# Optimization experiments

Hardware: AMD Instinct MI355X
Metric: run time of the kernel (lower is better)

The kernel has to match this reference:

```python
import jax, jax.numpy as jnp
import numpy as np

# DeepSeek MLA prefill pipeline (absorbed form), matching the GEMM/bmm/sparse-attention
# Dims: m=512 tokens, hidden=7168, d_kv_c=512, d_q_c=1536, d_r=64, d_q=d_kv=128,
# h=16 local heads, attention dim d = d_kv_c + d_r = 576, s_kv=4096, topk=512.

M, HID = 512, 7168
D_KV_C, D_Q_C, D_R, D_Q, D_KV = 512, 1536, 64, 128, 128
H = 16
S_KV, TOPK = 4096, 512
D_ATT = D_KV_C + D_R  # 576


def setup_inputs() -> dict:
    key = jax.random.key(0)
    ks = jax.random.split(key, 8)
    s = lambda n: 1.0 / np.sqrt(n).astype(np.float32)
    return {
        "x": jax.random.normal(ks[0], (M, HID), jnp.float32),
        "W_cqkv": jax.random.normal(ks[1], (HID, D_KV_C + D_Q_C + D_R), jnp.float32) * s(HID),
        "W_uq": jax.random.normal(ks[2], (D_Q_C, H * (D_Q + D_R)), jnp.float32) * s(D_Q_C),
        "W_qk": jax.random.normal(ks[3], (H, D_Q, D_KV_C), jnp.float32) * s(D_Q),
        "kv_cache": jax.random.normal(ks[4], (S_KV, D_ATT), jnp.float32),
        "W_o1": jax.random.normal(ks[5], (H, D_KV_C, D_KV), jnp.float32) * s(D_KV_C),
        "W_oproj": jax.random.normal(ks[6], (H * D_KV, HID), jnp.float32) * s(H * D_KV),
        "indices": jax.random.randint(ks[7], (M, TOPK), 0, S_KV, jnp.int32),
    }


def reference(x, W_cqkv, W_uq, W_qk, kv_cache, W_o1, W_oproj, indices):
    # 1) QKV compression GEMM: [m, hid] @ [hid, d_kv_c + d_q_c + d_r]
    c = x @ W_cqkv
    kv_c_new = c[:, :D_KV_C]                      # compressed KV (would extend cache)
    q_c = c[:, D_KV_C:D_KV_C + D_Q_C]             # [m, d_q_c]
    # (kv_c_new / k_r_new feed the cache in a real pipeline; attention below reads

    # 2) Q uncompression GEMM: [m, d_q_c] @ [d_q_c, h*(d_q+d_r)]
    q = (q_c @ W_uq).reshape(M, H, D_Q + D_R)
    q_nope, q_pe = q[..., :D_Q], q[..., D_Q:]     # [m,h,128], [m,h,64]

    # 3) Q absorb bmm: per-head [m, d_q] @ [d_q, d_kv_c]
    q_abs = jnp.einsum('mhq,hqc->mhc', q_nope, W_qk)
    q_full = jnp.concatenate([q_abs, q_pe], axis=-1)  # [m, h, 576]

    # 4) Top-k sparse MLA attention (flash_mla_sparse_fwd math):
    #    indices shared across heads (h_kv = 1); gather kv rows per query token.
    kv_g = kv_cache[indices]                      # [m, topk, 576]
    sm_scale = 1.0 / jnp.sqrt(jnp.float32(D_ATT))
    scores = jnp.einsum('mhd,mtd->mht', q_full, kv_g) * sm_scale
    attn = jax.nn.softmax(scores, axis=-1)        # [m, h, topk]
    o = jnp.einsum('mht,mtc->mhc', attn, kv_g[..., :D_KV_C])  # value = first d_kv_c dims

    # 5) O bmm: per-head [m, d_kv_c] @ [d_kv_c, d_kv]
    o2 = jnp.einsum('mhc,hcv->mhv', o, W_o1)      # [m, h, 128]

    # 6) O projection GEMM: [m, h*d_kv] @ [h*d_kv, hid]
    out = o2.reshape(M, H * D_KV) @ W_oproj       # [m, hid]
    return out
```

## Files before the change

kernel.cpp:

```cpp
#include <hip/hip_runtime.h>
#include <hip/hip_bf16.h>

#define M_DIM 512
#define HID 7168
#define D_KV_C 512
#define D_Q_C 1536
#define D_R 64
#define D_Q 128
#define D_KV 128
#define H_DIM 16
#define S_KV 4096
#define TOPK 512
#define D_ATT 576

typedef _Float16 half_t;
typedef __attribute__((ext_vector_type(8))) _Float16 f16x8_t;
typedef __attribute__((ext_vector_type(4))) float f32x4_t;
typedef __attribute__((ext_vector_type(2))) unsigned int u32x2_t;

#define MFMA_F16(a, b, c) __builtin_amdgcn_mfma_f32_16x16x32_f16((a), (b), (c), 0, 0, 0)

__device__ __forceinline__ unsigned lds_addr32(const void* p) {
    return (unsigned)(unsigned long long)(const __attribute__((address_space(3))) char*)p;
}

typedef const __attribute__((address_space(1))) unsigned int* gptr_t;
typedef __attribute__((address_space(3))) unsigned int* lptr_t;
__device__ __forceinline__ void gload_lds16(const void* g, void* l) {
    __builtin_amdgcn_global_load_lds((gptr_t)g, (lptr_t)l, 16, 0, 0);
}

__global__ __launch_bounds__(256) void cvt_f16(const float* __restrict__ src,
                                               half_t* __restrict__ dst, int n8)
{
    int i = blockIdx.x * 256 + threadIdx.x;
    if (i >= n8) return;
    const float4* s = (const float4*)src + (size_t)i * 2;
    float4 a = s[0], b = s[1];
    f16x8_t o;
    o[0] = (half_t)a.x; o[1] = (half_t)a.y; o[2] = (half_t)a.z; o[3] = (half_t)a.w;
    o[4] = (half_t)b.x; o[5] = (half_t)b.y; o[6] = (half_t)b.z; o[7] = (half_t)b.w;
    *(f16x8_t*)(dst + (size_t)i * 8) = o;
}

__global__ __launch_bounds__(256) void cvt_t(
    const float* __restrict__ src, int ld_src, long long sS,
    half_t* __restrict__ dst, int ld_dst, long long sD)
{
    src += (size_t)blockIdx.z * sS;
    dst += (size_t)blockIdx.z * sD;
    int k0 = blockIdx.y * 64, n0 = blockIdx.x * 64;
    __shared__ half_t t[64][80];
    int tid = threadIdx.x;
    int kr = tid >> 4, nc = (tid & 15) * 4;
    #pragma unroll
    for (int i = 0; i < 4; i++) {
        float4 v = *(const float4*)&src[(size_t)(k0 + kr + i * 16) * ld_src + n0 + nc];
        t[nc + 0][kr + i * 16] = (half_t)v.x;
        t[nc + 1][kr + i * 16] = (half_t)v.y;
        t[nc + 2][kr + i * 16] = (half_t)v.z;
        t[nc + 3][kr + i * 16] = (half_t)v.w;
    }
    __syncthreads();
    int nr = tid >> 2, kc = (tid & 3) * 16;
    f16x8_t w0 = *(const f16x8_t*)&t[nr][kc];
    f16x8_t w1 = *(const f16x8_t*)&t[nr][kc + 8];
    *(f16x8_t*)&dst[(size_t)(n0 + nr) * ld_dst + k0 + kc] = w0;
    *(f16x8_t*)&dst[(size_t)(n0 + nr) * ld_dst + k0 + kc + 8] = w1;
}

template<bool F16OUT>
__global__ __launch_bounds__(256) void gemm_f16t(
    const half_t* __restrict__ A, int lda, long long sA,
    const half_t* __restrict__ Bt, int ldb, long long sB,
    void* __restrict__ Cv, int ldc, long long sC, int K)
{
    A  += (size_t)blockIdx.z * sA;
    Bt += (size_t)blockIdx.z * sB;
    const int bm = blockIdx.y * 64, bn = blockIdx.x * 64;

    __shared__ __align__(16) char lds[2][16384];

    const int tid = threadIdx.x, w = tid >> 6, lane = tid & 63;
    const int l15 = lane & 15, q = lane >> 4;
    const int wr = w >> 1, wc = w & 1;

    const half_t* gA[2];
    const half_t* gB[2];
    #pragma unroll
    for (int p = 0; p < 2; p++) {
        int c = p * 64 + lane;
        int rl = c >> 3;
        int sg = (c & 7) ^ (rl & 7);
        gA[p] = A  + (size_t)(bm + w * 16 + rl) * lda + sg * 8;
        gB[p] = Bt + (size_t)(bn + w * 16 + rl) * ldb + sg * 8;
    }

    f32x4_t acc[2][2];
    #pragma unroll
    for (int i = 0; i < 2; i++)
        #pragma unroll
        for (int j = 0; j < 2; j++) acc[i][j] = (f32x4_t){0.f, 0.f, 0.f, 0.f};

    const int nsteps = K >> 6;

    {
        char* ab = lds[0];
        char* bb = ab + 8192;
        #pragma unroll
        for (int p = 0; p < 2; p++) {
            gload_lds16(gA[p], ab + w * 2048 + p * 1024);
            gload_lds16(gB[p], bb + w * 2048 + p * 1024);
        }
    }
    __syncthreads();

    int cur = 0;
    for (int s = 0; s < nsteps; s++) {
        if (s + 1 < nsteps) {
            int k0 = (s + 1) << 6;
            char* ab = lds[cur ^ 1];
            char* bb = ab + 8192;
            #pragma unroll
            for (int p = 0; p < 2; p++) {
                gload_lds16(gA[p] + k0, ab + w * 2048 + p * 1024);
                gload_lds16(gB[p] + k0, bb + w * 2048 + p * 1024);
            }
        }
        {
            const char* ab = lds[cur];
            const char* bb = ab + 8192;
            #pragma unroll
            for (int kk = 0; kk < 2; kk++) {
                f16x8_t av[2], bv[2];
                #pragma unroll
                for (int i = 0; i < 2; i++) {
                    int ra = wr * 32 + i * 16 + l15;
                    av[i] = *(const f16x8_t*)(ab + ra * 128 + (((kk * 4 + q) ^ (ra & 7)) * 16));
                    int rb = wc * 32 + i * 16 + l15;
                    bv[i] = *(const f16x8_t*)(bb + rb * 128 + (((kk * 4 + q) ^ (rb & 7)) * 16));
                }
                #pragma unroll
                for (int i = 0; i < 2; i++)
                    #pragma unroll
                    for (int j = 0; j < 2; j++)
                        acc[i][j] = MFMA_F16(av[i], bv[j], acc[i][j]);
            }
        }
        __syncthreads();
        cur ^= 1;
    }

    half_t* Ch = (half_t*)Cv + (F16OUT ? (size_t)blockIdx.z * sC : 0);
    float*  Cf = (float*)Cv  + (F16OUT ? 0 : (size_t)blockIdx.z * sC);
    #pragma unroll
    for (int i = 0; i < 2; i++)
        #pragma unroll
        for (int j = 0; j < 2; j++)
            #pragma unroll
            for (int r = 0; r < 4; r++) {
                size_t row = bm + wr * 32 + i * 16 + q * 4 + r;
                size_t col = bn + wc * 32 + j * 16 + l15;
                if (F16OUT) Ch[row * ldc + col] = (half_t)acc[i][j][r];
                else        Cf[row * ldc + col] = acc[i][j][r];
            }
}

__global__ void copy_pe16(const half_t* __restrict__ q, half_t* __restrict__ qf)
{
    int i = blockIdx.x * 256 + threadIdx.x;
    if (i >= M_DIM * H_DIM * D_R) return;
    int r = i & 63, mh = i >> 6;
    qf[(size_t)mh * D_ATT + D_KV_C + r] = q[(size_t)mh * (D_Q + D_R) + D_Q + r];
}

__global__ __launch_bounds__(256) void attn_mfma(
    const half_t* __restrict__ qf,
    const half_t* __restrict__ kvb,
    const int* __restrict__ indices,
    half_t* __restrict__ o)
{
    const int m = blockIdx.x;
    const int tid = threadIdx.x;
    const int w = tid >> 6, lane = tid & 63;
    const int l15 = lane & 15, q = lane >> 4;

    __shared__ __align__(16) char u_mem[16 * 513 * 4];
    __shared__ __align__(16) unsigned short p_s[16 * 512];
    __shared__ int idx_s[TOPK];

    float* s_s = (float*)u_mem;
    unsigned short* v_s = (unsigned short*)u_mem;

    for (int i = tid; i < TOPK; i += 256) idx_s[i] = indices[(size_t)m * TOPK + i];
    __syncthreads();

    int rows[8];
    #pragma unroll
    for (int tt = 0; tt < 8; tt++) rows[tt] = idx_s[(w * 8 + tt) * 16 + l15];

    f32x4_t acc[8];
    #pragma unroll
    for (int tt = 0; tt < 8; tt++) acc[tt] = (f32x4_t){0.f, 0.f, 0.f, 0.f};

    const half_t* qh = qf + ((size_t)m * 16 + l15) * D_ATT + q * 8;

    #pragma unroll 2
    for (int kk = 0; kk < 18; kk++) {
        f16x8_t ah = *(const f16x8_t*)(qh + kk * 32);
        #pragma unroll
        for (int tt = 0; tt < 8; tt++) {
            f16x8_t b = *(const f16x8_t*)(kvb + (size_t)rows[tt] * D_ATT + kk * 32 + q * 8);
            acc[tt] = MFMA_F16(ah, b, acc[tt]);
        }
    }

    const float scale = 1.0f / 24.0f;
    #pragma unroll
    for (int tt = 0; tt < 8; tt++) {
        int t = (w * 8 + tt) * 16 + l15;
        #pragma unroll
        for (int r = 0; r < 4; r++)
            s_s[(q * 4 + r) * 513 + t] = acc[tt][r] * scale;
    }
    __syncthreads();

    {
        int h = tid >> 4, j = tid & 15;
        float mx = -1e30f;
        for (int t = j; t < TOPK; t += 16) mx = fmaxf(mx, s_s[h * 513 + t]);
        #pragma unroll
        for (int off = 8; off; off >>= 1) mx = fmaxf(mx, __shfl_xor(mx, off, 16));
        float sum = 0.f;
        for (int t = j; t < TOPK; t += 16) {
            float e = __expf(s_s[h * 513 + t] - mx);
            s_s[h * 513 + t] = e;
            sum += e;
        }
        #pragma unroll
        for (int off = 8; off; off >>= 1) sum += __shfl_xor(sum, off, 16);
        float inv = 1.0f / sum;
        for (int t = j; t < TOPK; t += 16) {
            union { half_t h; unsigned short u; } cv;
            cv.h = (half_t)(s_s[h * 513 + t] * inv);
            unsigned byte = ((unsigned)(t * 2)) ^ (((unsigned)(h & 7)) << 4);
            p_s[h * 512 + (byte >> 1)] = cv.u;
        }
    }
    __syncthreads();

    f32x4_t oacc[8];
    #pragma unroll
    for (int i = 0; i < 8; i++) oacc[i] = (f32x4_t){0.f, 0.f, 0.f, 0.f};

    const unsigned vbase = lds_addr32(v_s);
    const int jb = tid & 7, trow = tid >> 3;
    const unsigned swz_w = (((unsigned)(trow & 7)) << 4) ^ (((unsigned)((trow >> 3) & 3)) << 5);

    const int row1 = q * 8 + (l15 >> 2);
    const int row2 = row1 + 4;
    const unsigned sw1 = (((unsigned)(row1 & 7)) << 4) ^ (((unsigned)q & 3u) << 5);
    const unsigned sw2 = (((unsigned)(row2 & 7)) << 4) ^ (((unsigned)q & 3u) << 5);
    const unsigned cbyte = (unsigned)((l15 & 3) * 8);

    #pragma unroll 1
    for (int ct = 0; ct < 16; ct++) {
        int t0 = ct * 32;
        {
            int r = idx_s[t0 + trow];
            const half_t* src = kvb + (size_t)r * D_ATT + jb * 64;
            #pragma unroll
            for (int i = 0; i < 8; i++) {
                unsigned byte = ((unsigned)(jb * 128 + i * 16)) ^ swz_w;
                *(f16x8_t*)((char*)v_s + trow * 1024 + byte) = *(const f16x8_t*)(src + i * 8);
            }
        }
        __syncthreads();

        f16x8_t pa;
        {
            unsigned pbyte = ((unsigned)(t0 * 2 + q * 16)) ^ (((unsigned)(l15 & 7)) << 4);
            pa = *(const f16x8_t*)((const char*)p_s + l15 * 1024 + pbyte);
        }

        u32x2_t blo[8], bhi[8];
        #pragma unroll
        for (int i = 0; i < 8; i++) {
            unsigned c2 = ((unsigned)(((w * 8 + i) * 16) * 2)) + cbyte;
            unsigned a1 = vbase + (unsigned)row1 * 1024u + (c2 ^ sw1);
            unsigned a2 = vbase + (unsigned)row2 * 1024u + (c2 ^ sw2);
            asm volatile("ds_read_b64_tr_b16 %0, %1 offset:0" : "=v"(blo[i]) : "v"(a1) : "memory");
            asm volatile("ds_read_b64_tr_b16 %0, %1 offset:0" : "=v"(bhi[i]) : "v"(a2) : "memory");
        }
        asm volatile("s_waitcnt lgkmcnt(0)" ::: "memory");
        __builtin_amdgcn_sched_barrier(0);

        #pragma unroll
        for (int i = 0; i < 8; i++) {
            union { f16x8_t s; struct { u32x2_t lo, hi; } u; } f;
            f.u.lo = blo[i]; f.u.hi = bhi[i];
            oacc[i] = MFMA_F16(pa, f.s, oacc[i]);
        }
        __syncthreads();
    }

    half_t* ob = o + (size_t)m * (H_DIM * D_KV_C);
    #pragma unroll
    for (int i = 0; i < 8; i++) {
        int c = (w * 8 + i) * 16 + l15;
        #pragma unroll
        for (int r = 0; r < 4; r++)
            ob[(size_t)(q * 4 + r) * D_KV_C + c] = (half_t)oacc[i][r];
    }
}

extern "C" void kernel_launch(void* const* d_in, const int* in_sizes, int n_in,
                              void* d_out, int out_size, void* d_ws, size_t ws_size,
                              hipStream_t stream)
{
    const float* x        = (const float*)d_in[0];
    const float* W_cqkv   = (const float*)d_in[1];
    const float* W_uq     = (const float*)d_in[2];
    const float* W_qk     = (const float*)d_in[3];
    const float* kv_cache = (const float*)d_in[4];
    const float* W_o1     = (const float*)d_in[5];
    const float* W_oproj  = (const float*)d_in[6];
    const int*   indices  = (const int*)d_in[7];
    float* out = (float*)d_out;

    half_t* wsh = (half_t*)d_ws;
    half_t* Wcqkv_t = wsh;
    half_t* o16     = wsh;
    half_t* Wuq_t   = wsh + 11010048;
    half_t* qf16    = wsh + 11010048;
    half_t* Wqk_t   = wsh + 15728640;
    half_t* Wo1_t   = wsh + 16777216;
    half_t* Wop_t   = wsh + 17825792;
    half_t* x16     = wsh + 32505856;
    half_t* o2_16   = wsh + 32505856;
    half_t* qc16    = wsh + 36175872;
    half_t* q16     = wsh + 36962304;
    half_t* kv16    = wsh + 38535168;

    cvt_f16<<<(M_DIM * HID / 8 + 255) / 256, 256, 0, stream>>>(x, x16, M_DIM * HID / 8);
    cvt_f16<<<(S_KV * D_ATT / 8 + 255) / 256, 256, 0, stream>>>(kv_cache, kv16, S_KV * D_ATT / 8);
    cvt_t<<<dim3(D_Q_C / 64, HID / 64, 1), 256, 0, stream>>>(
        W_cqkv + D_KV_C, D_KV_C + D_Q_C + D_R, 0, Wcqkv_t, HID, 0);
    cvt_t<<<dim3(3072 / 64, D_Q_C / 64, 1), 256, 0, stream>>>(
        W_uq, 3072, 0, Wuq_t, D_Q_C, 0);
    cvt_t<<<dim3(D_KV_C / 64, D_Q / 64, H_DIM), 256, 0, stream>>>(
        W_qk, D_KV_C, D_Q * D_KV_C, Wqk_t, D_Q, D_Q * D_KV_C);
    cvt_t<<<dim3(D_KV / 64, D_KV_C / 64, H_DIM), 256, 0, stream>>>(
        W_o1, D_KV, D_KV_C * D_KV, Wo1_t, D_KV_C, D_KV_C * D_KV);
    cvt_t<<<dim3(HID / 64, 2048 / 64, 1), 256, 0, stream>>>(
        W_oproj, HID, 0, Wop_t, 2048, 0);

    gemm_f16t<true><<<dim3(D_Q_C / 64, M_DIM / 64, 1), 256, 0, stream>>>(
        x16, HID, 0, Wcqkv_t, HID, 0, qc16, D_Q_C, 0, HID);

    gemm_f16t<true><<<dim3(3072 / 64, M_DIM / 64, 1), 256, 0, stream>>>(
        qc16, D_Q_C, 0, Wuq_t, D_Q_C, 0, q16, 3072, 0, D_Q_C);

    copy_pe16<<<(M_DIM * H_DIM * D_R + 255) / 256, 256, 0, stream>>>(q16, qf16);

    gemm_f16t<true><<<dim3(D_KV_C / 64, M_DIM / 64, H_DIM), 256, 0, stream>>>(
        q16, 3072, D_Q + D_R, Wqk_t, D_Q, (long long)D_Q * D_KV_C,
        qf16, H_DIM * D_ATT, D_ATT, D_Q);

    attn_mfma<<<M_DIM, 256, 0, stream>>>(qf16, kv16, indices, o16);

    gemm_f16t<true><<<dim3(D_KV / 64, M_DIM / 64, H_DIM), 256, 0, stream>>>(
        o16, H_DIM * D_KV_C, D_KV_C, Wo1_t, D_KV_C, (long long)D_KV_C * D_KV,
        o2_16, H_DIM * D_KV, D_KV, D_KV_C);

    gemm_f16t<false><<<dim3(HID / 64, M_DIM / 64, 1), 256, 0, stream>>>(
        o2_16, H_DIM * D_KV, 0, Wop_t, 2048, 0, out, HID, 0, H_DIM * D_KV);
}
```

Baseline: 261.4 us.

## Split-K the Q GEMMs with fused reduce, and prefetch KV rows in attention

Splits the QKV compression GEMM into 4 K-slices and the Q uncompression GEMM into 2. Each slice writes fp32 partials, and new reduction kernels sum them and convert to fp16. The second reduction also writes the rope part of q into qf, which replaces the copy_pe16 kernel. The point is to fill more CUs than the small 8x24 and 8x48 grids can. In attention, the next tile's gathered KV rows are loaded into registers during the current MFMAs, with MFMA priority raised, to hide gather latency. The cost is extra fp32 partial traffic, more register pressure, and a reshuffled workspace layout.

```diff
diff --git a/kernel.cpp b/kernel.cpp
--- a/kernel.cpp
+++ b/kernel.cpp
@@ -41,6 +41,52 @@
     o[0] = (half_t)a.x; o[1] = (half_t)a.y; o[2] = (half_t)a.z; o[3] = (half_t)a.w;
     o[4] = (half_t)b.x; o[5] = (half_t)b.y; o[6] = (half_t)b.z; o[7] = (half_t)b.w;
     *(f16x8_t*)(dst + (size_t)i * 8) = o;
+}
+
+template<int NS>
+__global__ __launch_bounds__(256) void cvt_sum(const float* __restrict__ src, long long slice,
+                                               half_t* __restrict__ dst, int n8)
+{
+    int i = blockIdx.x * 256 + threadIdx.x;
+    if (i >= n8) return;
+    float a[8] = {};
+    #pragma unroll
+    for (int s = 0; s < NS; s++) {
+        const float4* p = (const float4*)(src + (size_t)s * slice) + (size_t)i * 2;
+        float4 u = p[0], v = p[1];
+        a[0] += u.x; a[1] += u.y; a[2] += u.z; a[3] += u.w;
+        a[4] += v.x; a[5] += v.y; a[6] += v.z; a[7] += v.w;
+    }
+    f16x8_t o;
+    #pragma unroll
+    for (int j = 0; j < 8; j++) o[j] = (half_t)a[j];
+    *(f16x8_t*)(dst + (size_t)i * 8) = o;
+}
+
+__global__ __launch_bounds__(256) void cvt_sum_q(const float* __restrict__ src, long long slice,
+                                                 half_t* __restrict__ q16, half_t* __restrict__ qf)
+{
+    int i = blockIdx.x * 256 + threadIdx.x;
+    if (i >= M_DIM * 3072 / 8) return;
+    float a[8] = {};
+    #pragma unroll
+    for (int s = 0; s < 2; s++) {
+        const float4* p = (const float4*)(src + (size_t)s * slice) + (size_t)i * 2;
+        float4 u = p[0], v = p[1];
+        a[0] += u.x; a[1] += u.y; a[2] += u.z; a[3] += u.w;
+        a[4] += v.x; a[5] += v.y; a[6] += v.z; a[7] += v.w;
+    }
+    f16x8_t o;
+    #pragma unroll
+    for (int j = 0; j < 8; j++) o[j] = (half_t)a[j];
+    *(f16x8_t*)(q16 + (size_t)i * 8) = o;
+    int col = (i * 8) % 3072;
+    int c = col % 192;
+    if (c >= 128) {
+        int row = (i * 8) / 3072, h = col / 192;
+        int mh = row * 16 + h;
+        *(f16x8_t*)(qf + (size_t)mh * D_ATT + D_KV_C + (c - 128)) = o;
+    }
 }
 
 __global__ __launch_bounds__(256) void cvt_t(
@@ -166,14 +212,6 @@
             }
 }
 
-__global__ void copy_pe16(const half_t* __restrict__ q, half_t* __restrict__ qf)
-{
-    int i = blockIdx.x * 256 + threadIdx.x;
-    if (i >= M_DIM * H_DIM * D_R) return;
-    int r = i & 63, mh = i >> 6;
-    qf[(size_t)mh * D_ATT + D_KV_C + r] = q[(size_t)mh * (D_Q + D_R) + D_Q + r];
-}
-
 __global__ __launch_bounds__(256) void attn_mfma(
     const half_t* __restrict__ qf,
     const half_t* __restrict__ kvb,
@@ -257,25 +295,39 @@
     const int jb = tid & 7, trow = tid >> 3;
     const unsigned swz_w = (((unsigned)(trow & 7)) << 4) ^ (((unsigned)((trow >> 3) & 3)) << 5);
 
+    int rstage[16];
+    #pragma unroll
+    for (int ct = 0; ct < 16; ct++) rstage[ct] = idx_s[ct * 32 + trow];
+
     const int row1 = q * 8 + (l15 >> 2);
     const int row2 = row1 + 4;
     const unsigned sw1 = (((unsigned)(row1 & 7)) << 4) ^ (((unsigned)q & 3u) << 5);
     const unsigned sw2 = (((unsigned)(row2 & 7)) << 4) ^ (((unsigned)q & 3u) << 5);
     const unsigned cbyte = (unsigned)((l15 & 3) * 8);
 
+    {
+        const half_t* src = kvb + (size_t)rstage[0] * D_ATT + jb * 64;
+        f16x8_t tmp[8];
+        #pragma unroll
+        for (int i = 0; i < 8; i++) tmp[i] = *(const f16x8_t*)(src + i * 8);
+        #pragma unroll
+        for (int i = 0; i < 8; i++) {
+            unsigned byte = ((unsigned)(jb * 128 + i * 16)) ^ swz_w;
+            *(f16x8_t*)((char*)v_s + trow * 1024 + byte) = tmp[i];
+        }
+    }
+    __syncthreads();
+
     #pragma unroll 1
     for (int ct = 0; ct < 16; ct++) {
         int t0 = ct * 32;
-        {
-            int r = idx_s[t0 + trow];
-            const half_t* src = kvb + (size_t)r * D_ATT + jb * 64;
+
+        f16x8_t nxt[8];
+        if (ct < 15) {
+            const half_t* src = kvb + (size_t)rstage[ct + 1] * D_ATT + jb * 64;
             #pragma unroll
-            for (int i = 0; i < 8; i++) {
-                unsigned byte = ((unsigned)(jb * 128 + i * 16)) ^ swz_w;
-                *(f16x8_t*)((char*)v_s + trow * 1024 + byte) = *(const f16x8_t*)(src + i * 8);
-            }
-        }
-        __syncthreads();
+            for (int i = 0; i < 8; i++) nxt[i] = *(const f16x8_t*)(src + i * 8);
+        }
 
         f16x8_t pa;
         {
@@ -295,11 +347,23 @@
         asm volatile("s_waitcnt lgkmcnt(0)" ::: "memory");
         __builtin_amdgcn_sched_barrier(0);
 
+        __builtin_amdgcn_s_setprio(1);
         #pragma unroll
         for (int i = 0; i < 8; i++) {
             union { f16x8_t s; struct { u32x2_t lo, hi; } u; } f;
             f.u.lo = blo[i]; f.u.hi = bhi[i];
             oacc[i] = MFMA_F16(pa, f.s, oacc[i]);
+        }
+        __builtin_amdgcn_s_setprio(0);
+
+        __syncthreads();
+
+        if (ct < 15) {
+            #pragma unroll
+            for (int i = 0; i < 8; i++) {
+                unsigned byte = ((unsigned)(jb * 128 + i * 16)) ^ swz_w;
+                *(f16x8_t*)((char*)v_s + trow * 1024 + byte) = nxt[i];
+            }
         }
         __syncthreads();
     }
@@ -330,17 +394,21 @@
 
     half_t* wsh = (half_t*)d_ws;
     half_t* Wcqkv_t = wsh;
-    half_t* o16     = wsh;
-    half_t* Wuq_t   = wsh + 11010048;
-    half_t* qf16    = wsh + 11010048;
-    half_t* Wqk_t   = wsh + 15728640;
-    half_t* Wo1_t   = wsh + 16777216;
-    half_t* Wop_t   = wsh + 17825792;
-    half_t* x16     = wsh + 32505856;
-    half_t* o2_16   = wsh + 32505856;
-    half_t* qc16    = wsh + 36175872;
-    half_t* q16     = wsh + 36962304;
-    half_t* kv16    = wsh + 38535168;
+    half_t* qc16    = wsh;
+    half_t* q32h    = wsh + 786432;
+    half_t* q16     = wsh + 7077888;
+    half_t* x16     = wsh + 11010048;
+    half_t* o2_16   = wsh + 11010048;
+    half_t* Wuq_t   = wsh + 14680064;
+    half_t* o16     = wsh + 14680064;
+    half_t* Wqk_t   = wsh + 19398656;
+    half_t* Wo1_t   = wsh + 20447232;
+    half_t* Wop_t   = wsh + 21495808;
+    half_t* kv16    = wsh + 36175872;
+    half_t* qc32h   = wsh + 38535168;
+    half_t* qf16    = wsh + 38535168;
+    float* qc32 = (float*)qc32h;
+    float* q32  = (float*)q32h;
 
     cvt_f16<<<(M_DIM * HID / 8 + 255) / 256, 256, 0, stream>>>(x, x16, M_DIM * HID / 8);
     cvt_f16<<<(S_KV * D_ATT / 8 + 255) / 256, 256, 0, stream>>>(kv_cache, kv16, S_KV * D_ATT / 8);
@@ -355,13 +423,15 @@
     cvt_t<<<dim3(HID / 64, 2048 / 64, 1), 256, 0, stream>>>(
         W_oproj, HID, 0, Wop_t, 2048, 0);
 
-    gemm_f16t<true><<<dim3(D_Q_C / 64, M_DIM / 64, 1), 256, 0, stream>>>(
-        x16, HID, 0, Wcqkv_t, HID, 0, qc16, D_Q_C, 0, HID);
-
-    gemm_f16t<true><<<dim3(3072 / 64, M_DIM / 64, 1), 256, 0, stream>>>(
-        qc16, D_Q_C, 0, Wuq_t, D_Q_C, 0, q16, 3072, 0, D_Q_C);
-
-    copy_pe16<<<(M_DIM * H_DIM * D_R + 255) / 256, 256, 0, stream>>>(q16, qf16);
+    gemm_f16t<false><<<dim3(D_Q_C / 64, M_DIM / 64, 4), 256, 0, stream>>>(
+        x16, HID, 1792, Wcqkv_t, HID, 1792, qc32, D_Q_C, (long long)M_DIM * D_Q_C, 1792);
+    cvt_sum<4><<<(M_DIM * D_Q_C / 8 + 255) / 256, 256, 0, stream>>>(
+        qc32, (long long)M_DIM * D_Q_C, qc16, M_DIM * D_Q_C / 8);
+
+    gemm_f16t<false><<<dim3(3072 / 64, M_DIM / 64, 2), 256, 0, stream>>>(
+        qc16, D_Q_C, 768, Wuq_t, D_Q_C, 768, q32, 3072, (long long)M_DIM * 3072, 768);
+    cvt_sum_q<<<(M_DIM * 3072 / 8 + 255) / 256, 256, 0, stream>>>(
+        q32, (long long)M_DIM * 3072, q16, qf16);
 
     gemm_f16t<true><<<dim3(D_KV_C / 64, M_DIM / 64, H_DIM), 256, 0, stream>>>(
         q16, 3072, D_Q + D_R, Wqk_t, D_Q, (long long)D_Q * D_KV_C,
```

New measurement: 221.4 us. 1.18x faster.
